# Kernel optimization log

Measured on AMD Instinct MI355X. Metric: run time of the kernel, lower is better.

The kernel has to match this reference:

```python
import jax, jax.numpy as jnp
import numpy as np

LN2 = float(np.log(2.0))

def ssp(x):
    # ShiftedSoftplus: softplus(x) - log(2)
    return jax.nn.softplus(x) - LN2

N_NODES = 40000
N_EDGES = 640000
HIDDEN = 128
N_FILTERS = 128
N_GAUSS = 50
CUTOFF = 10.0

def setup_inputs() -> dict:
    key = jax.random.key(0)
    ks = jax.random.split(key, 12)
    s = 0.05
    x = jax.random.normal(ks[0], (N_NODES, HIDDEN), dtype=jnp.float32)
    edge_index = jax.random.randint(ks[1], (2, N_EDGES), 0, N_NODES)
    edge_weight = jax.random.uniform(ks[2], (N_EDGES,), dtype=jnp.float32) * CUTOFF
    edge_attr = jax.random.normal(ks[3], (N_EDGES, N_GAUSS), dtype=jnp.float32)
    # filter MLP params (Linear(num_gaussians,num_filters), ssp, Linear(num_filters,num_filters))
    mlp_w1 = jax.random.normal(ks[4], (N_FILTERS, N_GAUSS), dtype=jnp.float32) * s
    mlp_b1 = jnp.zeros((N_FILTERS,), dtype=jnp.float32)
    mlp_w2 = jax.random.normal(ks[5], (N_FILTERS, N_FILTERS), dtype=jnp.float32) * s
    mlp_b2 = jnp.zeros((N_FILTERS,), dtype=jnp.float32)
    # CFConv linears: lin1 (no bias), lin2 (bias)
    lin1_w = jax.random.normal(ks[6], (N_FILTERS, HIDDEN), dtype=jnp.float32) * s
    lin2_w = jax.random.normal(ks[7], (HIDDEN, N_FILTERS), dtype=jnp.float32) * s
    lin2_b = jnp.zeros((HIDDEN,), dtype=jnp.float32)
    # output linear
    lin_w = jax.random.normal(ks[8], (HIDDEN, HIDDEN), dtype=jnp.float32) * s
    lin_b = jnp.zeros((HIDDEN,), dtype=jnp.float32)
    return {
        "x": x, "edge_index": edge_index, "edge_weight": edge_weight, "edge_attr": edge_attr,
        "mlp_w1": mlp_w1, "mlp_b1": mlp_b1, "mlp_w2": mlp_w2, "mlp_b2": mlp_b2,
        "lin1_w": lin1_w, "lin2_w": lin2_w, "lin2_b": lin2_b,
        "lin_w": lin_w, "lin_b": lin_b,
    }

def reference(x, edge_index, edge_weight, edge_attr,
              mlp_w1, mlp_b1, mlp_w2, mlp_b2,
              lin1_w, lin2_w, lin2_b, lin_w, lin_b):
    src, dst = edge_index[0], edge_index[1]
    # cosine envelope
    C = 0.5 * (jnp.cos(edge_weight * jnp.pi / CUTOFF) + 1.0)  # (E,)
    # filter MLP on Gaussian-smeared distances
    W = ssp(edge_attr @ mlp_w1.T + mlp_b1) @ mlp_w2.T + mlp_b2  # (E, F)
    W = W * C[:, None]
    # CFConv: lin1 -> gather x_j -> multiply -> scatter-add -> lin2
    h = x @ lin1_w.T                                            # (N, F)
    msg = h[src] * W                                            # (E, F)
    agg = jax.ops.segment_sum(msg, dst, num_segments=x.shape[0])  # (N, F)
    h2 = agg @ lin2_w.T + lin2_b                                # (N, H)
    # activation + output projection
    out = ssp(h2) @ lin_w.T + lin_b                             # (N, H)
    return out
```

## Files before the change

kernel.cpp:

```cpp
#include <hip/hip_runtime.h>
#include <math.h>

#define LN2F 0.69314718055994531f

typedef _Float16 v8hf __attribute__((ext_vector_type(8)));
typedef float    v4f  __attribute__((ext_vector_type(4)));

__device__ __forceinline__ float ssp_fast(float x) {
    float e = __expf(-fabsf(x));
    return fmaxf(x, 0.f) + __logf(1.f + e) - LN2F;
}

__global__ __launch_bounds__(256)
void prep_kernel(const float* __restrict__ w1, const float* __restrict__ w2,
                 const float* __restrict__ l1w, const float* __restrict__ l2w,
                 const float* __restrict__ lw,
                 _Float16* __restrict__ w1f, _Float16* __restrict__ w2f,
                 _Float16* __restrict__ l1f, _Float16* __restrict__ l2f,
                 _Float16* __restrict__ lwf)
{
    int idx = blockIdx.x * 256 + threadIdx.x;
    if (idx < 8192) {
        int i = idx & 7, lane = (idx >> 3) & 63, ks = (idx >> 9) & 1, nt = idx >> 10;
        int r = nt * 16 + (lane & 15);
        int k = ks * 32 + (lane >> 4) * 8 + i;
        w1f[idx] = (k < 50) ? (_Float16)w1[r * 50 + k] : (_Float16)0.f;
        return;
    }
    int o = idx - 8192;
    if (o >= 4 * 16384) return;
    int which = o >> 14;
    int p = o & 16383;
    int i = p & 7, lane = (p >> 3) & 63, ks = (p >> 9) & 3, nt = p >> 11;
    int r = nt * 16 + (lane & 15);
    int k = ks * 32 + (lane >> 4) * 8 + i;
    const float* src = (which == 0) ? w2 : (which == 1) ? l1w : (which == 2) ? l2w : lw;
    _Float16* dst   = (which == 0) ? w2f : (which == 1) ? l1f : (which == 2) ? l2f : lwf;
    dst[p] = (_Float16)src[r * 128 + k];
}

__global__ __launch_bounds__(256)
void h_gemm_kernel(const float* __restrict__ X, const _Float16* __restrict__ Wf,
                   float* __restrict__ Y, int M)
{
    const int tid = threadIdx.x, lane = tid & 63, wv = tid >> 6;
    const int l15 = lane & 15, quad = lane >> 4;
    const int mb = blockIdx.x * 64 + wv * 16;
    const int nt0 = blockIdx.y * 4;

    const int mA = (mb + l15 < M) ? (mb + l15) : (M - 1);
    v8hf a[4];
    #pragma unroll
    for (int ks = 0; ks < 4; ++ks) {
        const float4* xp = (const float4*)&X[(size_t)mA * 128 + ks * 32 + quad * 8];
        float4 x0 = xp[0], x1 = xp[1];
        v8hf t = {(_Float16)x0.x, (_Float16)x0.y, (_Float16)x0.z, (_Float16)x0.w,
                  (_Float16)x1.x, (_Float16)x1.y, (_Float16)x1.z, (_Float16)x1.w};
        a[ks] = t;
    }
    #pragma unroll
    for (int nt = nt0; nt < nt0 + 4; ++nt) {
        v4f acc = {0.f, 0.f, 0.f, 0.f};
        #pragma unroll
        for (int ks = 0; ks < 4; ++ks) {
            const v8hf b = *(const v8hf*)&Wf[((nt * 4 + ks) * 64 + lane) * 8];
            acc = __builtin_amdgcn_mfma_f32_16x16x32_f16(a[ks], b, acc, 0, 0, 0);
        }
        const int col = nt * 16 + l15;
        #pragma unroll
        for (int r = 0; r < 4; ++r) {
            int row = mb + quad * 4 + r;
            if (row < M) Y[(size_t)row * 128 + col] = acc[r];
        }
    }
}

__global__ __launch_bounds__(256)
void fused_out_kernel(const float* __restrict__ agg, const _Float16* __restrict__ l2f,
                      const float* __restrict__ l2b, const _Float16* __restrict__ lwf,
                      const float* __restrict__ lb, float* __restrict__ out, int M)
{
    __shared__ __align__(16) _Float16 Sh[64 * 138];
    const int tid = threadIdx.x, lane = tid & 63, wv = tid >> 6;
    const int l15 = lane & 15, quad = lane >> 4;
    const int m0 = wv * 16;
    const int gbase = blockIdx.x * 64;
    const int nt0 = blockIdx.y * 4;

    const int mA = (gbase + m0 + l15 < M) ? (gbase + m0 + l15) : (M - 1);
    v8hf a[4];
    #pragma unroll
    for (int ks = 0; ks < 4; ++ks) {
        const float4* xp = (const float4*)&agg[(size_t)mA * 128 + ks * 32 + quad * 8];
        float4 x0 = xp[0], x1 = xp[1];
        v8hf t = {(_Float16)x0.x, (_Float16)x0.y, (_Float16)x0.z, (_Float16)x0.w,
                  (_Float16)x1.x, (_Float16)x1.y, (_Float16)x1.z, (_Float16)x1.w};
        a[ks] = t;
    }
    #pragma unroll
    for (int nt = 0; nt < 8; ++nt) {
        v4f acc = {0.f, 0.f, 0.f, 0.f};
        #pragma unroll
        for (int ks = 0; ks < 4; ++ks) {
            const v8hf b = *(const v8hf*)&l2f[((nt * 4 + ks) * 64 + lane) * 8];
            acc = __builtin_amdgcn_mfma_f32_16x16x32_f16(a[ks], b, acc, 0, 0, 0);
        }
        const float bj = l2b[nt * 16 + l15];
        #pragma unroll
        for (int r = 0; r < 4; ++r)
            Sh[(m0 + quad * 4 + r) * 138 + nt * 16 + l15] =
                (_Float16)ssp_fast(acc[r] + bj);
    }
    v8hf ua[4];
    #pragma unroll
    for (int ks = 0; ks < 4; ++ks)
        ua[ks] = *(const v8hf*)&Sh[(m0 + l15) * 138 + ks * 32 + quad * 8];

    #pragma unroll
    for (int nt = nt0; nt < nt0 + 4; ++nt) {
        v4f acc = {0.f, 0.f, 0.f, 0.f};
        #pragma unroll
        for (int ks = 0; ks < 4; ++ks) {
            const v8hf b = *(const v8hf*)&lwf[((nt * 4 + ks) * 64 + lane) * 8];
            acc = __builtin_amdgcn_mfma_f32_16x16x32_f16(ua[ks], b, acc, 0, 0, 0);
        }
        const int col = nt * 16 + l15;
        const float bj = lb[col];
        #pragma unroll
        for (int r = 0; r < 4; ++r) {
            int row = gbase + m0 + quad * 4 + r;
            if (row < M) out[(size_t)row * 128 + col] = acc[r] + bj;
        }
    }
}

__global__ __launch_bounds__(256, 7)
void edge_kernel(const float* __restrict__ attr,
                 const float* __restrict__ ew,
                 const int* __restrict__ srcI,
                 const int* __restrict__ dstI,
                 const _Float16* __restrict__ w1f,
                 const _Float16* __restrict__ w2f,
                 const float* __restrict__ b1,
                 const float* __restrict__ b2,
                 const float* __restrict__ h,
                 float* __restrict__ agg,
                 int E)
{
    __shared__ __align__(16) _Float16 Uh[64 * 138];

    const int tid = threadIdx.x;
    const int e_base = blockIdx.x * 64;
    const int lane = tid & 63, wv = tid >> 6;
    const int m0 = wv * 16, l15 = lane & 15, quad = lane >> 4;

    float cC[4]; const float* hrow[4]; float* arow[4]; bool val[4];
    #pragma unroll
    for (int r = 0; r < 4; ++r) {
        int eg = e_base + m0 + quad * 4 + r;
        val[r] = eg < E;
        int e = val[r] ? eg : (E - 1);
        cC[r] = 0.5f * (__cosf(ew[e] * 0.31415926535897932f) + 1.f);
        hrow[r] = h + (size_t)srcI[e] * 128;
        arow[r] = agg + (size_t)dstI[e] * 128;
    }

    int ar = e_base + m0 + l15;
    if (ar >= E) ar = E - 1;
    const float* rp = attr + (size_t)ar * 50;
    v8hf a0, a1;
    {
        const float2 q0 = *(const float2*)(rp + quad * 8 + 0);
        const float2 q1 = *(const float2*)(rp + quad * 8 + 2);
        const float2 q2 = *(const float2*)(rp + quad * 8 + 4);
        const float2 q3 = *(const float2*)(rp + quad * 8 + 6);
        v8hf t = {(_Float16)q0.x, (_Float16)q0.y, (_Float16)q1.x, (_Float16)q1.y,
                  (_Float16)q2.x, (_Float16)q2.y, (_Float16)q3.x, (_Float16)q3.y};
        a0 = t;
    }
    {
        const int cb = 32 + quad * 8;
        float2 q[4];
        #pragma unroll
        for (int j = 0; j < 4; ++j) {
            const int c = cb + 2 * j;
            if (c < 50) q[j] = *(const float2*)(rp + c);
            else        { q[j].x = 0.f; q[j].y = 0.f; }
        }
        v8hf t = {(_Float16)q[0].x, (_Float16)q[0].y, (_Float16)q[1].x, (_Float16)q[1].y,
                  (_Float16)q[2].x, (_Float16)q[2].y, (_Float16)q[3].x, (_Float16)q[3].y};
        a1 = t;
    }

    float hv[8][4];
    #pragma unroll
    for (int nt = 0; nt < 8; ++nt)
        #pragma unroll
        for (int r = 0; r < 4; ++r)
            hv[nt][r] = hrow[r][nt * 16 + l15];

    #pragma unroll
    for (int nt = 0; nt < 8; ++nt) {
        v4f acc = {0.f, 0.f, 0.f, 0.f};
        const v8hf bA = *(const v8hf*)&w1f[((nt * 2 + 0) * 64 + lane) * 8];
        const v8hf bB = *(const v8hf*)&w1f[((nt * 2 + 1) * 64 + lane) * 8];
        acc = __builtin_amdgcn_mfma_f32_16x16x32_f16(a0, bA, acc, 0, 0, 0);
        acc = __builtin_amdgcn_mfma_f32_16x16x32_f16(a1, bB, acc, 0, 0, 0);
        const float bj = b1[nt * 16 + l15];
        #pragma unroll
        for (int r = 0; r < 4; ++r)
            Uh[(m0 + quad * 4 + r) * 138 + nt * 16 + l15] =
                (_Float16)ssp_fast(acc[r] + bj);
    }

    v8hf ua[4];
    #pragma unroll
    for (int ks = 0; ks < 4; ++ks)
        ua[ks] = *(const v8hf*)&Uh[(m0 + l15) * 138 + ks * 32 + quad * 8];

    #pragma unroll
    for (int nt = 0; nt < 8; ++nt) {
        v4f acc = {0.f, 0.f, 0.f, 0.f};
        #pragma unroll
        for (int ks = 0; ks < 4; ++ks) {
            const v8hf b = *(const v8hf*)&w2f[((nt * 4 + ks) * 64 + lane) * 8];
            acc = __builtin_amdgcn_mfma_f32_16x16x32_f16(ua[ks], b, acc, 0, 0, 0);
        }
        const int col = nt * 16 + l15;
        const float bj = b2[col];
        #pragma unroll
        for (int r = 0; r < 4; ++r) {
            if (val[r]) {
                float wf = (acc[r] + bj) * cC[r];
                atomicAdd(&arow[r][col], wf * hv[nt][r]);
            }
        }
    }
}

extern "C" void kernel_launch(void* const* d_in, const int* in_sizes, int n_in,
                              void* d_out, int out_size, void* d_ws, size_t ws_size,
                              hipStream_t stream)
{
    const float* x   = (const float*)d_in[0];
    const int*   ei  = (const int*)  d_in[1];
    const float* ew  = (const float*)d_in[2];
    const float* ea  = (const float*)d_in[3];
    const float* w1  = (const float*)d_in[4];
    const float* b1  = (const float*)d_in[5];
    const float* w2  = (const float*)d_in[6];
    const float* b2  = (const float*)d_in[7];
    const float* l1w = (const float*)d_in[8];
    const float* l2w = (const float*)d_in[9];
    const float* l2b = (const float*)d_in[10];
    const float* lw  = (const float*)d_in[11];
    const float* lb  = (const float*)d_in[12];

    const int N = in_sizes[0] / 128;
    const int E = in_sizes[2];

    float* hbuf = (float*)d_ws;
    float* agg  = hbuf + (size_t)N * 128;
    _Float16* w1f = (_Float16*)(agg + (size_t)N * 128);
    _Float16* w2f = w1f + 8192;
    _Float16* l1f = w2f + 16384;
    _Float16* l2f = l1f + 16384;
    _Float16* lwf = l2f + 16384;

    const int nb = (N + 63) / 64;
    const int eb = (E + 63) / 64;

    prep_kernel<<<288, 256, 0, stream>>>(w1, w2, l1w, l2w, lw,
                                         w1f, w2f, l1f, l2f, lwf);
    hipMemsetAsync(agg, 0, (size_t)N * 128 * sizeof(float), stream);
    h_gemm_kernel<<<dim3(nb, 2), 256, 0, stream>>>(x, l1f, hbuf, N);
    edge_kernel<<<eb, 256, 0, stream>>>(ea, ew, ei, ei + E, w1f, w2f, b1, b2,
                                        hbuf, agg, E);
    fused_out_kernel<<<dim3(nb, 2), 256, 0, stream>>>(agg, l2f, l2b, lwf, lb,
                                                      (float*)d_out, N);
}
```

Baseline: 543.4 us.

## Sort edges by source node via counting sort before edge kernel

Adds a histogram, two-pass scan and atomic ranking pass that group edges by source index, then permutes src, dst, the cosine envelope and fp16-packed edge attributes into sorted order. The edge kernel then reads these contiguous, pre-converted arrays, so the h[src] gathers hit neighbouring rows and get better cache reuse. The cost is several extra kernels each call, including a full rewrite of the 640k x 50 attribute array, plus atomic contention in the ranking pass.

```diff
diff --git a/kernel.cpp b/kernel.cpp
--- a/kernel.cpp
+++ b/kernel.cpp
@@ -134,11 +134,103 @@
     }
 }
 
+__global__ __launch_bounds__(256)
+void hist_kernel(const int* __restrict__ key, int* __restrict__ counts, int E)
+{
+    int i = blockIdx.x * 256 + threadIdx.x;
+    const int stride = gridDim.x * 256;
+    for (; i < E; i += stride) atomicAdd(&counts[key[i]], 1);
+}
+
+__global__ __launch_bounds__(256)
+void scan1_kernel(int* __restrict__ data, int* __restrict__ bsum, int N)
+{
+    __shared__ int wsum[4];
+    const int t = threadIdx.x, lane = t & 63, wv = t >> 6;
+    const int base = blockIdx.x * 1024 + t * 4;
+    int v0 = 0, v1 = 0, v2 = 0, v3 = 0;
+    if (base + 0 < N) v0 = data[base + 0];
+    if (base + 1 < N) v1 = data[base + 1];
+    if (base + 2 < N) v2 = data[base + 2];
+    if (base + 3 < N) v3 = data[base + 3];
+    const int s = v0 + v1 + v2 + v3;
+    int sc = s;
+    #pragma unroll
+    for (int d = 1; d < 64; d <<= 1) {
+        int o = __shfl_up(sc, d);
+        if (lane >= d) sc += o;
+    }
+    if (lane == 63) wsum[wv] = sc;
+    __syncthreads();
+    int wo = 0;
+    for (int j = 0; j < wv; ++j) wo += wsum[j];
+    int run = wo + (sc - s);
+    if (base + 0 < N) data[base + 0] = run; run += v0;
+    if (base + 1 < N) data[base + 1] = run; run += v1;
+    if (base + 2 < N) data[base + 2] = run; run += v2;
+    if (base + 3 < N) data[base + 3] = run; run += v3;
+    if (t == 255) bsum[blockIdx.x] = wo + sc;
+}
+
+__global__ __launch_bounds__(256)
+void scan2_kernel(int* __restrict__ offs, const int* __restrict__ bsum,
+                  int* __restrict__ cur, int N, int E)
+{
+    int add = 0;
+    for (int j = 0; j < (int)blockIdx.x; ++j) add += bsum[j];
+    const int base = blockIdx.x * 1024 + threadIdx.x * 4;
+    #pragma unroll
+    for (int r = 0; r < 4; ++r) {
+        int i = base + r;
+        if (i < N) { int o = offs[i] + add; offs[i] = o; cur[i] = o; }
+    }
+    if (blockIdx.x == 0 && threadIdx.x == 0) offs[N] = E;
+}
+
+__global__ __launch_bounds__(256)
+void rank_perm_kernel(const int* __restrict__ src, const int* __restrict__ dst,
+                      const float* __restrict__ ew, int* __restrict__ cur,
+                      int* __restrict__ rank, int* __restrict__ srcP,
+                      int* __restrict__ dstP, float* __restrict__ cCP, int E)
+{
+    int i = blockIdx.x * 256 + threadIdx.x;
+    const int stride = gridDim.x * 256;
+    for (; i < E; i += stride) {
+        const int s = src[i];
+        const int p = atomicAdd(&cur[s], 1);
+        rank[i] = p;
+        srcP[p] = s;
+        dstP[p] = dst[i];
+        cCP[p] = 0.5f * (__cosf(ew[i] * 0.31415926535897932f) + 1.f);
+    }
+}
+
+__global__ __launch_bounds__(256)
+void attr_perm_kernel(const float* __restrict__ attr, const int* __restrict__ rank,
+                      _Float16* __restrict__ attrP, int E)
+{
+    int idx = blockIdx.x * 256 + threadIdx.x;
+    const int stride = gridDim.x * 256;
+    const int total = E * 8;
+    for (; idx < total; idx += stride) {
+        const int e = idx >> 3, sub = idx & 7;
+        const int p = rank[e];
+        const float* rp = attr + (size_t)e * 50 + sub * 8;
+        v8hf t;
+        #pragma unroll
+        for (int j = 0; j < 8; ++j) {
+            const int c = sub * 8 + j;
+            t[j] = (c < 50) ? (_Float16)rp[j] : (_Float16)0.f;
+        }
+        *(v8hf*)&attrP[(size_t)p * 64 + sub * 8] = t;
+    }
+}
+
 __global__ __launch_bounds__(256, 7)
-void edge_kernel(const float* __restrict__ attr,
-                 const float* __restrict__ ew,
-                 const int* __restrict__ srcI,
-                 const int* __restrict__ dstI,
+void edge_kernel(const _Float16* __restrict__ attrP,
+                 const float* __restrict__ cCP,
+                 const int* __restrict__ srcP,
+                 const int* __restrict__ dstP,
                  const _Float16* __restrict__ w1f,
                  const _Float16* __restrict__ w2f,
                  const float* __restrict__ b1,
@@ -154,43 +246,34 @@
     const int lane = tid & 63, wv = tid >> 6;
     const int m0 = wv * 16, l15 = lane & 15, quad = lane >> 4;
 
+    const int s0 = e_base + m0 + quad * 4;
     float cC[4]; const float* hrow[4]; float* arow[4]; bool val[4];
-    #pragma unroll
-    for (int r = 0; r < 4; ++r) {
-        int eg = e_base + m0 + quad * 4 + r;
-        val[r] = eg < E;
-        int e = val[r] ? eg : (E - 1);
-        cC[r] = 0.5f * (__cosf(ew[e] * 0.31415926535897932f) + 1.f);
-        hrow[r] = h + (size_t)srcI[e] * 128;
-        arow[r] = agg + (size_t)dstI[e] * 128;
-    }
-
-    int ar = e_base + m0 + l15;
-    if (ar >= E) ar = E - 1;
-    const float* rp = attr + (size_t)ar * 50;
-    v8hf a0, a1;
-    {
-        const float2 q0 = *(const float2*)(rp + quad * 8 + 0);
-        const float2 q1 = *(const float2*)(rp + quad * 8 + 2);
-        const float2 q2 = *(const float2*)(rp + quad * 8 + 4);
-        const float2 q3 = *(const float2*)(rp + quad * 8 + 6);
-        v8hf t = {(_Float16)q0.x, (_Float16)q0.y, (_Float16)q1.x, (_Float16)q1.y,
-                  (_Float16)q2.x, (_Float16)q2.y, (_Float16)q3.x, (_Float16)q3.y};
-        a0 = t;
-    }
-    {
-        const int cb = 32 + quad * 8;
-        float2 q[4];
-        #pragma unroll
-        for (int j = 0; j < 4; ++j) {
-            const int c = cb + 2 * j;
-            if (c < 50) q[j] = *(const float2*)(rp + c);
-            else        { q[j].x = 0.f; q[j].y = 0.f; }
-        }
-        v8hf t = {(_Float16)q[0].x, (_Float16)q[0].y, (_Float16)q[1].x, (_Float16)q[1].y,
-                  (_Float16)q[2].x, (_Float16)q[2].y, (_Float16)q[3].x, (_Float16)q[3].y};
-        a1 = t;
-    }
+    if (s0 + 3 < E) {
+        const float4 c4 = *(const float4*)&cCP[s0];
+        const int4  sv = *(const int4*)&srcP[s0];
+        const int4  dv = *(const int4*)&dstP[s0];
+        cC[0] = c4.x; cC[1] = c4.y; cC[2] = c4.z; cC[3] = c4.w;
+        hrow[0] = h + (size_t)sv.x * 128; hrow[1] = h + (size_t)sv.y * 128;
+        hrow[2] = h + (size_t)sv.z * 128; hrow[3] = h + (size_t)sv.w * 128;
+        arow[0] = agg + (size_t)dv.x * 128; arow[1] = agg + (size_t)dv.y * 128;
+        arow[2] = agg + (size_t)dv.z * 128; arow[3] = agg + (size_t)dv.w * 128;
+        val[0] = val[1] = val[2] = val[3] = true;
+    } else {
+        #pragma unroll
+        for (int r = 0; r < 4; ++r) {
+            const int sg = s0 + r;
+            val[r] = sg < E;
+            const int s = val[r] ? sg : (E - 1);
+            cC[r] = cCP[s];
+            hrow[r] = h + (size_t)srcP[s] * 128;
+            arow[r] = agg + (size_t)dstP[s] * 128;
+        }
+    }
+
+    int sA = e_base + m0 + l15;
+    if (sA >= E) sA = E - 1;
+    const v8hf a0 = *(const v8hf*)&attrP[(size_t)sA * 64 + quad * 8];
+    const v8hf a1 = *(const v8hf*)&attrP[(size_t)sA * 64 + 32 + quad * 8];
 
     float hv[8][4];
     #pragma unroll
@@ -258,24 +341,50 @@
 
     const int N = in_sizes[0] / 128;
     const int E = in_sizes[2];
-
-    float* hbuf = (float*)d_ws;
-    float* agg  = hbuf + (size_t)N * 128;
-    _Float16* w1f = (_Float16*)(agg + (size_t)N * 128);
-    _Float16* w2f = w1f + 8192;
-    _Float16* l1f = w2f + 16384;
-    _Float16* l2f = l1f + 16384;
-    _Float16* lwf = l2f + 16384;
+    const int NB = (N + 1023) / 1024;
+
+    char* base = (char*)d_ws;
+    size_t off = 0;
+    auto take = [&](size_t bytes) -> char* {
+        char* r = base + off;
+        off = (off + bytes + 255) & ~(size_t)255;
+        return r;
+    };
+    float*    hbuf  = (float*)   take((size_t)N * 128 * 4);
+    float*    agg   = (float*)   take((size_t)N * 128 * 4);
+    _Float16* w1f   = (_Float16*)take(8192 * 2);
+    _Float16* w2f   = (_Float16*)take(16384 * 2);
+    _Float16* l1f   = (_Float16*)take(16384 * 2);
+    _Float16* l2f   = (_Float16*)take(16384 * 2);
+    _Float16* lwf   = (_Float16*)take(16384 * 2);
+    int*      offs  = (int*)     take((size_t)(N + 1) * 4);
+    int*      cur   = (int*)     take((size_t)N * 4);
+    int*      bsum  = (int*)     take((size_t)NB * 4);
+    int*      rank  = (int*)     take((size_t)E * 4);
+    int*      srcP  = (int*)     take((size_t)E * 4);
+    int*      dstP  = (int*)     take((size_t)E * 4);
+    float*    cCP   = (float*)   take((size_t)E * 4);
+    _Float16* attrP = (_Float16*)take((size_t)E * 64 * 2);
 
     const int nb = (N + 63) / 64;
     const int eb = (E + 63) / 64;
+    const int tb = (E + 255) / 256;
 
     prep_kernel<<<288, 256, 0, stream>>>(w1, w2, l1w, l2w, lw,
                                          w1f, w2f, l1f, l2f, lwf);
     hipMemsetAsync(agg, 0, (size_t)N * 128 * sizeof(float), stream);
+    hipMemsetAsync(offs, 0, (size_t)(N + 1) * sizeof(int), stream);
     h_gemm_kernel<<<dim3(nb, 2), 256, 0, stream>>>(x, l1f, hbuf, N);
-    edge_kernel<<<eb, 256, 0, stream>>>(ea, ew, ei, ei + E, w1f, w2f, b1, b2,
-                                        hbuf, agg, E);
+
+    hist_kernel<<<tb, 256, 0, stream>>>(ei, offs, E);
+    scan1_kernel<<<NB, 256, 0, stream>>>(offs, bsum, N);
+    scan2_kernel<<<NB, 256, 0, stream>>>(offs, bsum, cur, N, E);
+    rank_perm_kernel<<<tb, 256, 0, stream>>>(ei, ei + E, ew, cur,
+                                             rank, srcP, dstP, cCP, E);
+    attr_perm_kernel<<<(E * 8 + 255) / 256, 256, 0, stream>>>(ea, rank, attrP, E);
+
+    edge_kernel<<<eb, 256, 0, stream>>>(attrP, cCP, srcP, dstP, w1f, w2f,
+                                        b1, b2, hbuf, agg, E);
     fused_out_kernel<<<dim3(nb, 2), 256, 0, stream>>>(agg, l2f, l2b, lwf, lb,
                                                       (float*)d_out, N);
 }
```

Result: slower. 682.8 us (+25.7%).
